# Performance work log

Measured on AMD Instinct MI355X. Metric: run time of the kernel, lower is better.

The kernel has to match this reference:

```python
import jax, jax.numpy as jnp
import numpy as np

B, N, D = 4, 1024, 1024      # batch, seq_len, query_dim
H, DH = 16, 64               # heads, dim_head; inner = H*DH = 1024
INNER = H * DH
SCALE = DH ** -0.5


def setup_inputs() -> dict:
    key = jax.random.key(0)
    ks = jax.random.split(key, 8)
    x = jax.random.normal(ks[0], (B, N, D), dtype=jnp.float32)
    rel_pos = jax.random.normal(ks[1], (B * H, N, N), dtype=jnp.float32)
    query_mask = jax.random.randint(ks[2], (B, N), 0, 2).astype(bool)
    context_mask = jax.random.randint(ks[3], (B, N), 0, 2).astype(bool)
    # Linear weights stored (in, out); to_q/to_kv have no bias, to_out has bias.
    Wq = jax.random.normal(ks[4], (D, INNER), dtype=jnp.float32) / np.sqrt(D)
    Wkv = jax.random.normal(ks[5], (D, 2 * INNER), dtype=jnp.float32) / np.sqrt(D)
    Wo = jax.random.normal(ks[6], (INNER, D), dtype=jnp.float32) / np.sqrt(INNER)
    bo = jax.random.normal(ks[7], (D,), dtype=jnp.float32) * 0.01
    return {"x": x, "rel_pos": rel_pos, "query_mask": query_mask,
            "context_mask": context_mask, "Wq": Wq, "Wkv": Wkv, "Wo": Wo, "bo": bo}


def reference(x, rel_pos, query_mask, context_mask, Wq, Wkv, Wo, bo):
    # Self-attention (context = x)
    q = x @ Wq                                 # [B, N, INNER]
    kv = x @ Wkv                               # [B, N, 2*INNER]
    k, v = jnp.split(kv, 2, axis=-1)
    # (b n (h d)) -> (b h n d)
    split_heads = lambda t: t.reshape(B, N, H, DH).transpose(0, 2, 1, 3)
    q, k, v = map(split_heads, (q, k, v))
    sim = jnp.einsum('bhid,bhjd->bhij', q, k) * SCALE
    sim = sim + rel_pos.reshape(B, H, N, N)
    neg = -jnp.finfo(sim.dtype).max
    # query_mask: (b i) -> mask rows; context_mask: (b j) -> mask cols
    sim = jnp.where(query_mask[:, None, :, None], sim, neg)
    sim = jnp.where(context_mask[:, None, None, :], sim, neg)
    attn = jax.nn.softmax(sim, axis=-1)
    out = jnp.einsum('bhij,bhjd->bhid', attn, v)    # [B, H, N, DH]
    out = out.transpose(0, 2, 1, 3).reshape(B, N, INNER)
    return out @ Wo + bo
```

## Files before the change

kernel.cpp:

```cpp
#include <hip/hip_runtime.h>


#define NEGMAX 3.402823466e+38f

typedef short short8 __attribute__((ext_vector_type(8)));
typedef float f32x4 __attribute__((ext_vector_type(4)));

__device__ __forceinline__ unsigned short f2bf(float f) {
  unsigned int u = __float_as_uint(f);
  u += 0x7FFFu + ((u >> 16) & 1u);
  return (unsigned short)(u >> 16);
}

__device__ __forceinline__ void stage16(const void* g, void* lds_base, int lane) {
#if __has_builtin(__builtin_amdgcn_global_load_lds)
  __builtin_amdgcn_global_load_lds(
      (const __attribute__((address_space(1))) unsigned int*)g,
      (__attribute__((address_space(3))) unsigned int*)lds_base, 16, 0, 0);
#else
  *(int4*)((char*)lds_base + lane * 16) = *(const int4*)g;
#endif
}

__global__ void cast_x_k(const float* __restrict__ x, unsigned short* __restrict__ xb) {
  int i = (blockIdx.x * 256 + threadIdx.x) * 4;
  float4 v = *(const float4*)(x + i);
  ushort4 o;
  o.x = f2bf(v.x); o.y = f2bf(v.y); o.z = f2bf(v.z); o.w = f2bf(v.w);
  *(ushort4*)(xb + i) = o;
}

__global__ __launch_bounds__(256) void tcast_k(const float* __restrict__ src, int ldsrc,
                                               unsigned short* __restrict__ dst) {
  __shared__ float T[64][65];
  const int n0 = blockIdx.x * 64, d0 = blockIdx.y * 64;
  const int tx = threadIdx.x & 63, ty = threadIdx.x >> 6;
#pragma unroll
  for (int k = 0; k < 16; ++k) {
    int dl = k * 4 + ty;
    T[dl][tx] = src[(size_t)(d0 + dl) * ldsrc + n0 + tx];
  }
  __syncthreads();
#pragma unroll
  for (int k = 0; k < 16; ++k) {
    int nl = k * 4 + ty;
    dst[(size_t)(n0 + nl) * 1024 + d0 + tx] = f2bf(T[tx][nl]);
  }
}

__global__ __launch_bounds__(256) void gemm_bt_k(
    const unsigned short* __restrict__ A, const unsigned short* __restrict__ Bt,
    unsigned short* __restrict__ qws, unsigned short* __restrict__ kws,
    unsigned short* __restrict__ vtws) {
  constexpr int K = 1024;
  constexpr int NKB = K / 32;
  __shared__ alignas(16) unsigned short As[128 * 32];
  __shared__ alignas(16) unsigned short Bs[128 * 32];
  const int tid = threadIdx.x;
  const int lane = tid & 63, w = tid >> 6;
  const int quad = lane >> 4, lanelo = lane & 15;
  const int tRow = blockIdx.y * 128, tCol = blockIdx.x * 128;
  const int wr = (w >> 1) * 64, wc = (w & 1) * 64;
  const char* AgB = (const char*)(A + (size_t)tRow * K);
  const char* BgB = (const char*)(Bt + (size_t)tCol * K);
  const int c0 = tid, c1 = tid + 256;
  const size_t a0off = (size_t)(c0 >> 2) * 2048 + (c0 & 3) * 16;
  const size_t a1off = (size_t)(c1 >> 2) * 2048 + (c1 & 3) * 16;
  char* ldsA0 = (char*)As + w * 1024;
  char* ldsA1 = (char*)As + 4096 + w * 1024;
  char* ldsB0 = (char*)Bs + w * 1024;
  char* ldsB1 = (char*)Bs + 4096 + w * 1024;

  f32x4 acc[4][4];
#pragma unroll
  for (int i = 0; i < 4; ++i)
#pragma unroll
    for (int j = 0; j < 4; ++j) acc[i][j] = (f32x4){0.f, 0.f, 0.f, 0.f};

  for (int kb = 0; kb < NKB; ++kb) {
    if (kb) __syncthreads();
    const size_t ko = (size_t)kb * 64;
    stage16(AgB + a0off + ko, ldsA0, lane);
    stage16(AgB + a1off + ko, ldsA1, lane);
    stage16(BgB + a0off + ko, ldsB0, lane);
    stage16(BgB + a1off + ko, ldsB1, lane);
    __syncthreads();

    short8 af[4], bf[4];
#pragma unroll
    for (int i = 0; i < 4; ++i)
      af[i] = *(const short8*)(As + (wr + i * 16 + lanelo) * 32 + quad * 8);
#pragma unroll
    for (int j = 0; j < 4; ++j)
      bf[j] = *(const short8*)(Bs + (wc + j * 16 + lanelo) * 32 + quad * 8);
#pragma unroll
    for (int i = 0; i < 4; ++i)
#pragma unroll
      for (int j = 0; j < 4; ++j)
        acc[i][j] = __builtin_amdgcn_mfma_f32_16x16x32_bf16(af[i], bf[j], acc[i][j], 0, 0, 0);
  }

#pragma unroll
  for (int i = 0; i < 4; ++i) {
    int row = tRow + wr + i * 16 + quad * 4;
    int b_ = row >> 10;
    int npos = row & 1023;
#pragma unroll
    for (int j = 0; j < 4; ++j) {
      int col = tCol + wc + j * 16 + lanelo;
      if (col < 2048) {
        unsigned short* dst = (col < 1024) ? qws : kws;
        int c = col & 1023;
        int hh = c >> 6, dh = c & 63;
        size_t base = ((size_t)(b_ * 16 + hh) * 1024 + npos) * 64 + dh;
#pragma unroll
        for (int r = 0; r < 4; ++r) dst[base + (size_t)r * 64] = f2bf(acc[i][j][r]);
      } else {
        int c = col - 2048;
        ushort4 pk;
        pk.x = f2bf(acc[i][j][0]);
        pk.y = f2bf(acc[i][j][1]);
        pk.z = f2bf(acc[i][j][2]);
        pk.w = f2bf(acc[i][j][3]);
        *(ushort4*)&vtws[((size_t)(b_ * 16 + (c >> 6)) * 64 + (c & 63)) * 1024 + npos] = pk;
      }
    }
  }
}

__global__ __launch_bounds__(256) void gemm64_k(
    const unsigned short* __restrict__ A, const unsigned short* __restrict__ Bt,
    const float* __restrict__ bias, float* __restrict__ Cout) {
  constexpr int K = 1024;
  constexpr int NKB = K / 32;
  __shared__ alignas(16) unsigned short As[64 * 32];
  __shared__ alignas(16) unsigned short Bs[64 * 32];
  const int tid = threadIdx.x;
  const int lane = tid & 63, w = tid >> 6;
  const int quad = lane >> 4, lanelo = lane & 15;
  const int tRow = blockIdx.y * 64, tCol = blockIdx.x * 64;
  const char* AgB = (const char*)(A + (size_t)tRow * K);
  const char* BgB = (const char*)(Bt + (size_t)tCol * K);
  const size_t aoff = (size_t)(tid >> 2) * 2048 + (tid & 3) * 16;
  char* ldsA = (char*)As + w * 1024;
  char* ldsB = (char*)Bs + w * 1024;

  f32x4 acc[4];
#pragma unroll
  for (int j = 0; j < 4; ++j) acc[j] = (f32x4){0.f, 0.f, 0.f, 0.f};

  for (int kb = 0; kb < NKB; ++kb) {
    if (kb) __syncthreads();
    const size_t ko = (size_t)kb * 64;
    stage16(AgB + aoff + ko, ldsA, lane);
    stage16(BgB + aoff + ko, ldsB, lane);
    __syncthreads();

    short8 af = *(const short8*)(As + (w * 16 + lanelo) * 32 + quad * 8);
#pragma unroll
    for (int j = 0; j < 4; ++j) {
      short8 bf = *(const short8*)(Bs + (j * 16 + lanelo) * 32 + quad * 8);
      acc[j] = __builtin_amdgcn_mfma_f32_16x16x32_bf16(af, bf, acc[j], 0, 0, 0);
    }
  }

  const int row = tRow + w * 16 + quad * 4;
#pragma unroll
  for (int j = 0; j < 4; ++j) {
    int col = tCol + j * 16 + lanelo;
    float bv = bias[col];
#pragma unroll
    for (int r = 0; r < 4; ++r)
      Cout[(size_t)(row + r) * 1024 + col] = acc[j][r] + bv;
  }
}

__global__ __launch_bounds__(256, 4) void attn_k(
    const unsigned short* __restrict__ q_ws, const unsigned short* __restrict__ k_ws,
    const unsigned short* __restrict__ vt_ws, const float* __restrict__ rel,
    const int* __restrict__ qmask, const int* __restrict__ cmask,
    unsigned short* __restrict__ aout) {
  constexpr float SCALE = 0.125f;
  __shared__ alignas(16) unsigned short Pl[4 * 16 * 72];
  __shared__ float cml[1024];

  const int tid = threadIdx.x;
  const int w = tid >> 6, lane = tid & 63;
  const int quad = lane >> 4, lanelo = lane & 15;

  const int flat = blockIdx.y * 16 + blockIdx.x;
  const int virt = (flat & 7) * 128 + (flat >> 3);
  const int bh = virt >> 4, qblk = virt & 15;
  const int b_ = bh >> 4, h = bh & 15;
  const int qrow0 = qblk * 64 + w * 16;

  for (int i = tid; i < 1024; i += 256)
    cml[i] = (cmask[b_ * 1024 + i] != 0) ? 1.f : 0.f;
  __syncthreads();

  const unsigned short* qg = q_ws + ((size_t)bh * 1024 + qrow0) * 64;
  short8 qf0 = *(const short8*)(qg + (size_t)lanelo * 64 + quad * 8);
  short8 qf1 = *(const short8*)(qg + (size_t)lanelo * 64 + 32 + quad * 8);

  float qmv[4];
#pragma unroll
  for (int r = 0; r < 4; ++r)
    qmv[r] = (qmask[b_ * 1024 + qrow0 + quad * 4 + r] != 0) ? 1.f : 0.f;

  f32x4 o[4];
#pragma unroll
  for (int g = 0; g < 4; ++g) o[g] = (f32x4){0.f, 0.f, 0.f, 0.f};
  float m_run[4], l_run[4];
#pragma unroll
  for (int r = 0; r < 4; ++r) { m_run[r] = -NEGMAX; l_run[r] = 0.f; }

  const unsigned short* kg = k_ws + (size_t)bh * 65536;
  const unsigned short* vg = vt_ws + (size_t)bh * 65536;
  const float* relg = rel + ((size_t)bh * 1024 + qrow0) * 1024;
  unsigned short* pw = Pl + w * 16 * 72;

  float rl[4][4];
#pragma unroll
  for (int r = 0; r < 4; ++r)
#pragma unroll
    for (int c = 0; c < 4; ++c)
      rl[r][c] = relg[(size_t)(quad * 4 + r) * 1024 + c * 16 + lanelo];

  for (int kb = 0; kb < 16; ++kb) {
    const int key0 = kb * 64;

    f32x4 s[4];
#pragma unroll
    for (int c = 0; c < 4; ++c) {
      const unsigned short* krow = kg + (size_t)(key0 + c * 16 + lanelo) * 64;
      short8 kfa = *(const short8*)(krow + quad * 8);
      short8 kfb = *(const short8*)(krow + 32 + quad * 8);
      s[c] = (f32x4){0.f, 0.f, 0.f, 0.f};
      s[c] = __builtin_amdgcn_mfma_f32_16x16x32_bf16(qf0, kfa, s[c], 0, 0, 0);
      s[c] = __builtin_amdgcn_mfma_f32_16x16x32_bf16(qf1, kfb, s[c], 0, 0, 0);
    }

    float rln[4][4];
    if (kb + 1 < 16) {
#pragma unroll
      for (int r = 0; r < 4; ++r)
#pragma unroll
        for (int c = 0; c < 4; ++c)
          rln[r][c] = relg[(size_t)(quad * 4 + r) * 1024 + key0 + 64 + c * 16 + lanelo];
    }

    float cm[4];
#pragma unroll
    for (int c = 0; c < 4; ++c) cm[c] = cml[key0 + c * 16 + lanelo];

#pragma unroll
    for (int r = 0; r < 4; ++r) {
      const bool qok = qmv[r] != 0.f;
      float x[4], mloc = -NEGMAX;
#pragma unroll
      for (int c = 0; c < 4; ++c) {
        x[c] = (qok && cm[c] != 0.f) ? s[c][r] * SCALE + rl[r][c] : -NEGMAX;
        mloc = fmaxf(mloc, x[c]);
      }
      for (int off = 1; off < 16; off <<= 1) mloc = fmaxf(mloc, __shfl_xor(mloc, off));
      float mnew = fmaxf(m_run[r], mloc);
      float alpha = __expf(m_run[r] - mnew);
      m_run[r] = mnew;
      float ps = 0.f;
      unsigned short pb[4];
#pragma unroll
      for (int c = 0; c < 4; ++c) {
        float p = __expf(x[c] - mnew);
        ps += p;
        pb[c] = f2bf(p);
      }
      for (int off = 1; off < 16; off <<= 1) ps += __shfl_xor(ps, off);
      l_run[r] = l_run[r] * alpha + ps;
#pragma unroll
      for (int g = 0; g < 4; ++g) o[g][r] *= alpha;
#pragma unroll
      for (int c = 0; c < 4; ++c) pw[(quad * 4 + r) * 72 + c * 16 + lanelo] = pb[c];
    }

    if (kb + 1 < 16) {
#pragma unroll
      for (int r = 0; r < 4; ++r)
#pragma unroll
        for (int c = 0; c < 4; ++c) rl[r][c] = rln[r][c];
    }

#pragma unroll
    for (int c2 = 0; c2 < 2; ++c2) {
      short8 pa = *(const short8*)((const char*)pw + lanelo * 144 + c2 * 64 + quad * 16);
#pragma unroll
      for (int g = 0; g < 4; ++g) {
        short8 vb = *(const short8*)(vg + (size_t)(g * 16 + lanelo) * 1024 + key0 + c2 * 32 + quad * 8);
        o[g] = __builtin_amdgcn_mfma_f32_16x16x32_bf16(pa, vb, o[g], 0, 0, 0);
      }
    }
  }

#pragma unroll
  for (int r = 0; r < 4; ++r) {
    float inv = 1.f / l_run[r];
    size_t row = (size_t)(b_ * 1024 + qrow0 + quad * 4 + r) * 1024;
#pragma unroll
    for (int g = 0; g < 4; ++g)
      aout[row + h * 64 + g * 16 + lanelo] = f2bf(o[g][r] * inv);
  }
}

extern "C" void kernel_launch(void* const* d_in, const int* in_sizes, int n_in,
                              void* d_out, int out_size, void* d_ws, size_t ws_size,
                              hipStream_t stream) {
  const float* x = (const float*)d_in[0];
  const float* rel = (const float*)d_in[1];
  const int* qmask = (const int*)d_in[2];
  const int* cmask = (const int*)d_in[3];
  const float* Wq = (const float*)d_in[4];
  const float* Wkv = (const float*)d_in[5];
  const float* Wo = (const float*)d_in[6];
  const float* bo = (const float*)d_in[7];
  float* out = (float*)d_out;

  char* ws = (char*)d_ws;
  const size_t MB = 1024 * 1024;
  unsigned short* w3t = (unsigned short*)(ws);
  unsigned short* wot = (unsigned short*)(ws + 6 * MB);
  unsigned short* xb  = (unsigned short*)(ws + 8 * MB);
  unsigned short* qws = (unsigned short*)(ws + 16 * MB);
  unsigned short* kws = (unsigned short*)(ws + 24 * MB);
  unsigned short* vtws = (unsigned short*)(ws + 32 * MB);
  unsigned short* aout = xb;

  cast_x_k<<<4096, 256, 0, stream>>>(x, xb);
  tcast_k<<<dim3(16, 16), 256, 0, stream>>>(Wq, 1024, w3t);
  tcast_k<<<dim3(32, 16), 256, 0, stream>>>(Wkv, 2048, w3t + (size_t)1024 * 1024);
  tcast_k<<<dim3(16, 16), 256, 0, stream>>>(Wo, 1024, wot);
  gemm_bt_k<<<dim3(24, 32), 256, 0, stream>>>(xb, w3t, qws, kws, vtws);
  attn_k<<<dim3(16, 64), 256, 0, stream>>>(qws, kws, vtws, rel, qmask, cmask, aout);
  gemm64_k<<<dim3(16, 64), 256, 0, stream>>>(aout, wot, bo, out);
}
```

Before: 521.6 us.

## Stage K tiles into double-buffered swizzled LDS and prefetch V fragments early

K tiles for each 64-key block are now loaded cooperatively into a double-buffered, XOR-swizzled LDS buffer with direct global-to-LDS loads, one block ahead. Each wave previously read all K rows separately from global memory. V fragments are loaded at the top of each iteration so their latency overlaps the QK and softmax work, and the rel_pos prefetch moves to after the softmax. This adds 16KB of LDS and a barrier per iteration, which may lower occupancy and adds sync cost.

```diff
diff --git a/kernel.cpp b/kernel.cpp
--- a/kernel.cpp
+++ b/kernel.cpp
@@ -175,12 +175,15 @@
   }
 }
 
-__global__ __launch_bounds__(256, 4) void attn_k(
+__global__ __launch_bounds__(256)
+__attribute__((amdgpu_waves_per_eu(4, 4)))
+void attn_k(
     const unsigned short* __restrict__ q_ws, const unsigned short* __restrict__ k_ws,
     const unsigned short* __restrict__ vt_ws, const float* __restrict__ rel,
     const int* __restrict__ qmask, const int* __restrict__ cmask,
     unsigned short* __restrict__ aout) {
   constexpr float SCALE = 0.125f;
+  __shared__ alignas(16) unsigned short Kl[2 * 64 * 64];
   __shared__ alignas(16) unsigned short Pl[4 * 16 * 72];
   __shared__ float cml[1024];
 
@@ -194,31 +197,45 @@
   const int b_ = bh >> 4, h = bh & 15;
   const int qrow0 = qblk * 64 + w * 16;
 
-  for (int i = tid; i < 1024; i += 256)
-    cml[i] = (cmask[b_ * 1024 + i] != 0) ? 1.f : 0.f;
-  __syncthreads();
-
-  const unsigned short* qg = q_ws + ((size_t)bh * 1024 + qrow0) * 64;
-  short8 qf0 = *(const short8*)(qg + (size_t)lanelo * 64 + quad * 8);
-  short8 qf1 = *(const short8*)(qg + (size_t)lanelo * 64 + 32 + quad * 8);
-
-  float qmv[4];
-#pragma unroll
-  for (int r = 0; r < 4; ++r)
-    qmv[r] = (qmask[b_ * 1024 + qrow0 + quad * 4 + r] != 0) ? 1.f : 0.f;
-
-  f32x4 o[4];
-#pragma unroll
-  for (int g = 0; g < 4; ++g) o[g] = (f32x4){0.f, 0.f, 0.f, 0.f};
-  float m_run[4], l_run[4];
-#pragma unroll
-  for (int r = 0; r < 4; ++r) { m_run[r] = -NEGMAX; l_run[r] = 0.f; }
-
   const unsigned short* kg = k_ws + (size_t)bh * 65536;
   const unsigned short* vg = vt_ws + (size_t)bh * 65536;
   const float* relg = rel + ((size_t)bh * 1024 + qrow0) * 1024;
   unsigned short* pw = Pl + w * 16 * 72;
 
+  const int srow = lane >> 3;
+  const int sp = lane & 7;
+  const int spx = ((sp ^ srow) << 4);
+#define STAGE_K(buf, key0n)                                                     \
+  {                                                                             \
+    _Pragma("unroll")                                                           \
+    for (int i_ = 0; i_ < 2; ++i_) {                                            \
+      int row_ = w * 16 + i_ * 8 + srow;                                        \
+      stage16((const char*)kg + (size_t)((key0n) + row_) * 128 + spx,           \
+              (char*)Kl + (buf) * 8192 + w * 2048 + i_ * 1024, lane);           \
+    }                                                                           \
+  }
+
+  STAGE_K(0, 0);
+
+  for (int i = tid; i < 1024; i += 256)
+    cml[i] = (cmask[b_ * 1024 + i] != 0) ? 1.f : 0.f;
+
+  const unsigned short* qg = q_ws + ((size_t)bh * 1024 + qrow0) * 64;
+  short8 qf0 = *(const short8*)(qg + (size_t)lanelo * 64 + quad * 8);
+  short8 qf1 = *(const short8*)(qg + (size_t)lanelo * 64 + 32 + quad * 8);
+
+  float qmv[4];
+#pragma unroll
+  for (int r = 0; r < 4; ++r)
+    qmv[r] = (qmask[b_ * 1024 + qrow0 + quad * 4 + r] != 0) ? 1.f : 0.f;
+
+  f32x4 o[4];
+#pragma unroll
+  for (int g = 0; g < 4; ++g) o[g] = (f32x4){0.f, 0.f, 0.f, 0.f};
+  float m_run[4], l_run[4];
+#pragma unroll
+  for (int r = 0; r < 4; ++r) { m_run[r] = -NEGMAX; l_run[r] = 0.f; }
+
   float rl[4][4];
 #pragma unroll
   for (int r = 0; r < 4; ++r)
@@ -226,27 +243,33 @@
     for (int c = 0; c < 4; ++c)
       rl[r][c] = relg[(size_t)(quad * 4 + r) * 1024 + c * 16 + lanelo];
 
+  const int sb = lanelo & 7;
+
   for (int kb = 0; kb < 16; ++kb) {
     const int key0 = kb * 64;
+    const int cur = kb & 1;
+
+    __syncthreads();
+
+    if (kb + 1 < 16) STAGE_K(cur ^ 1, key0 + 64);
+
+    short8 vf[8];
+#pragma unroll
+    for (int c2 = 0; c2 < 2; ++c2)
+#pragma unroll
+      for (int g = 0; g < 4; ++g)
+        vf[c2 * 4 + g] = *(const short8*)(vg + (size_t)(g * 16 + lanelo) * 1024 +
+                                          key0 + c2 * 32 + quad * 8);
 
     f32x4 s[4];
 #pragma unroll
     for (int c = 0; c < 4; ++c) {
-      const unsigned short* krow = kg + (size_t)(key0 + c * 16 + lanelo) * 64;
-      short8 kfa = *(const short8*)(krow + quad * 8);
-      short8 kfb = *(const short8*)(krow + 32 + quad * 8);
+      const char* kbase = (const char*)Kl + cur * 8192 + (c * 16 + lanelo) * 128;
+      short8 kfa = *(const short8*)(kbase + ((quad ^ sb) << 4));
+      short8 kfb = *(const short8*)(kbase + (((4 + quad) ^ sb) << 4));
       s[c] = (f32x4){0.f, 0.f, 0.f, 0.f};
       s[c] = __builtin_amdgcn_mfma_f32_16x16x32_bf16(qf0, kfa, s[c], 0, 0, 0);
       s[c] = __builtin_amdgcn_mfma_f32_16x16x32_bf16(qf1, kfb, s[c], 0, 0, 0);
-    }
-
-    float rln[4][4];
-    if (kb + 1 < 16) {
-#pragma unroll
-      for (int r = 0; r < 4; ++r)
-#pragma unroll
-        for (int c = 0; c < 4; ++c)
-          rln[r][c] = relg[(size_t)(quad * 4 + r) * 1024 + key0 + 64 + c * 16 + lanelo];
     }
 
     float cm[4];
@@ -286,19 +309,19 @@
 #pragma unroll
       for (int r = 0; r < 4; ++r)
 #pragma unroll
-        for (int c = 0; c < 4; ++c) rl[r][c] = rln[r][c];
+        for (int c = 0; c < 4; ++c)
+          rl[r][c] = relg[(size_t)(quad * 4 + r) * 1024 + key0 + 64 + c * 16 + lanelo];
     }
 
 #pragma unroll
     for (int c2 = 0; c2 < 2; ++c2) {
       short8 pa = *(const short8*)((const char*)pw + lanelo * 144 + c2 * 64 + quad * 16);
 #pragma unroll
-      for (int g = 0; g < 4; ++g) {
-        short8 vb = *(const short8*)(vg + (size_t)(g * 16 + lanelo) * 1024 + key0 + c2 * 32 + quad * 8);
-        o[g] = __builtin_amdgcn_mfma_f32_16x16x32_bf16(pa, vb, o[g], 0, 0, 0);
-      }
-    }
-  }
+      for (int g = 0; g < 4; ++g)
+        o[g] = __builtin_amdgcn_mfma_f32_16x16x32_bf16(pa, vf[c2 * 4 + g], o[g], 0, 0, 0);
+    }
+  }
+#undef STAGE_K
 
 #pragma unroll
   for (int r = 0; r < 4; ++r) {
```

Measured after the change: 487.6 us. 1.07x faster.
